# Kernel optimization log

Hardware: AMD Instinct MI355X
Metric: run time of the kernel (lower is better)

The kernel has to match this reference:

```python
import jax, jax.numpy as jnp
import numpy as np

HIDDEN, KEY_DIM, VALUE_DIM = 1024, 1024, 1024
BATCH, SEQ = 8, 2048


def setup_inputs() -> dict:
    key = jax.random.key(0)
    ks = jax.random.split(key, 9)
    s = lambda fan_in: 1.0 / np.sqrt(fan_in)
    return {
        "y_all": jax.random.normal(ks[0], (BATCH, SEQ, HIDDEN), dtype=jnp.float32),
        # torch nn.Linear weights stored as (in, out) for x @ W + b
        "Wq": jax.random.uniform(ks[1], (HIDDEN, KEY_DIM), jnp.float32, -s(HIDDEN), s(HIDDEN)),
        "bq": jax.random.uniform(ks[2], (KEY_DIM,), jnp.float32, -s(HIDDEN), s(HIDDEN)),
        "Wk": jax.random.uniform(ks[3], (HIDDEN, KEY_DIM), jnp.float32, -s(HIDDEN), s(HIDDEN)),
        "bk": jax.random.uniform(ks[4], (KEY_DIM,), jnp.float32, -s(HIDDEN), s(HIDDEN)),
        "Wv": jax.random.uniform(ks[5], (HIDDEN, VALUE_DIM), jnp.float32, -s(HIDDEN), s(HIDDEN)),
        "bv": jax.random.uniform(ks[6], (VALUE_DIM,), jnp.float32, -s(HIDDEN), s(HIDDEN)),
        "Wo": jax.random.uniform(ks[7], (VALUE_DIM, HIDDEN), jnp.float32, -s(VALUE_DIM), s(VALUE_DIM)),
        "bo": jax.random.uniform(ks[8], (HIDDEN,), jnp.float32, -s(VALUE_DIM), s(VALUE_DIM)),
    }


def reference(y_all, Wq, bq, Wk, bk, Wv, bv, Wo, bo):
    # Original loops over t, each step attending last hidden state to the full
    # prefix. Equivalent to a single causal-masked attention pass.
    B, T, H = y_all.shape
    dk = Wq.shape[1]
    q = (y_all @ Wq + bq) / jnp.sqrt(jnp.asarray(dk, y_all.dtype))  # [B,T,dk]
    k = y_all @ Wk + bk                                              # [B,T,dk]
    v = y_all @ Wv + bv                                              # [B,T,dv]
    scores = jnp.einsum("bid,bjd->bij", q, k)                        # [B,T,T]
    causal = jnp.tril(jnp.ones((T, T), dtype=bool))                  # j <= i
    scores = jnp.where(causal, scores, -jnp.inf)
    weights = jax.nn.softmax(scores, axis=-1)
    ctx = jnp.einsum("bij,bjd->bid", weights, v)                     # [B,T,dv]
    return ctx @ Wo + bo                                             # [B,T,H]
```

## Files before the change

kernel.cpp:

```cpp
#include <hip/hip_runtime.h>

typedef __attribute__((ext_vector_type(8))) __bf16 bf16x8;
typedef __attribute__((ext_vector_type(4))) float f32x4;
typedef __attribute__((ext_vector_type(4))) float f4;
typedef __attribute__((ext_vector_type(4))) unsigned short ushort4_t;

__device__ inline void gload16(const void* g, void* l) {
  __builtin_amdgcn_global_load_lds(
      (const __attribute__((address_space(1))) unsigned int*)g,
      (__attribute__((address_space(3))) unsigned int*)l, 16, 0, 0);
}

__global__ void convert_bf16_k(const float* __restrict__ in, __bf16* __restrict__ out, int n8) {
  int i = blockIdx.x * blockDim.x + threadIdx.x;
  int stride = gridDim.x * blockDim.x;
  for (; i < n8; i += stride) {
    f4 a = ((const f4*)in)[2 * (long long)i];
    f4 b = ((const f4*)in)[2 * (long long)i + 1];
    bf16x8 o;
#pragma unroll
    for (int e = 0; e < 4; e++) { o[e] = (__bf16)a[e]; o[e + 4] = (__bf16)b[e]; }
    ((bf16x8*)out)[i] = o;
  }
}

__global__ void pack_bias_k(const float* __restrict__ bq, const float* __restrict__ bk,
                            const float* __restrict__ bv, float* __restrict__ out) {
  int i = blockIdx.x * 256 + threadIdx.x;
  if (i >= 3072) return;
  const float* src = (i < 1024) ? bq : (i < 2048) ? bk : bv;
  out[i] = src[i & 1023];
}

__global__ void transpose_w_k(const float* __restrict__ W0, const float* __restrict__ W1,
                              const float* __restrict__ W2, const float* __restrict__ W3,
                              __bf16* __restrict__ out) {
  int z = blockIdx.z;
  const float* W = (z == 0) ? W0 : (z == 1) ? W1 : (z == 2) ? W2 : W3;
  __bf16* O = out + (long long)z * 1048576;
  __shared__ float tile[32][33];
  int tx = threadIdx.x, ty = threadIdx.y;
  int n0 = blockIdx.x * 32, k0 = blockIdx.y * 32;
#pragma unroll
  for (int i = 0; i < 4; i++)
    tile[ty + i * 8][tx] = W[(long long)(k0 + ty + i * 8) * 1024 + n0 + tx];
  __syncthreads();
#pragma unroll
  for (int i = 0; i < 4; i++)
    O[(long long)(n0 + ty + i * 8) * 1024 + k0 + tx] = (__bf16)tile[tx][ty + i * 8];
}


#define LOADA(BASE, MIB)                                                       \
  _Pragma("unroll") for (int mi = 0; mi < 4; mi++)                             \
      _Pragma("unroll") for (int kh = 0; kh < 2; kh++) {                       \
    int row = ((MIB) + mi) * 16 + ln15;                                        \
    int pb = (row * 128 + (kh * 32 + kq * 8) * 2) ^ ((row & 7) << 4);          \
    a[mi][kh] = *(const bf16x8*)((BASE) + pb);                                 \
  }

#define LOADB(BASE, NIB)                                                       \
  _Pragma("unroll") for (int ni = 0; ni < 2; ni++)                             \
      _Pragma("unroll") for (int kh = 0; kh < 2; kh++) {                       \
    int row = brow0 + ((NIB) + ni) * 16 + ln15;                                \
    int pb = (row * 128 + (kh * 32 + kq * 8) * 2) ^ ((row & 7) << 4);          \
    b[(NIB) + ni][kh] = *(const bf16x8*)((BASE) + pb);                         \
  }

#define MFMAQ(MI0, NI0)                                                        \
  _Pragma("unroll") for (int mi = 0; mi < 4; mi++)                             \
      _Pragma("unroll") for (int ni = 0; ni < 2; ni++)                         \
          _Pragma("unroll") for (int kh = 0; kh < 2; kh++)                     \
              acc[(MI0) + mi][(NI0) + ni] =                                    \
      __builtin_amdgcn_mfma_f32_16x16x32_bf16(a[mi][kh], b[(NI0) + ni][kh],    \
                                              acc[(MI0) + mi][(NI0) + ni], 0, 0, 0);

#define FENCE asm volatile("" ::: "memory")

#define BARW                                           \
  FENCE;                                               \
  __builtin_amdgcn_s_barrier();                        \
  FENCE;                                               \
  __builtin_amdgcn_s_setprio(1);

#define ENDP                                           \
  __builtin_amdgcn_s_setprio(0);                       \
  FENCE;                                               \
  __builtin_amdgcn_s_barrier();                        \
  FENCE;

#define ENDPB                                          \
  __builtin_amdgcn_s_setprio(0);                       \
  asm volatile("s_waitcnt vmcnt(8)" ::: "memory");     \
  __builtin_amdgcn_s_barrier();                        \
  FENCE;

template <int OUT, int SWZ>
__global__ __launch_bounds__(512, 2) void gemm8(
    const __bf16* __restrict__ A0, int lda, long long sAz,
    const __bf16* __restrict__ B0, int ldb, long long sBz,
    void* __restrict__ C0v, int ldc, long long sCz,
    const float* __restrict__ bias0, int sBiasZ,
    float scale_z0, int k_tiles_base, int k_tiles_per_br,
    __bf16* __restrict__ vt_out) {
  int br, bc, z;
  {
    const int lin = (blockIdx.z * gridDim.y + blockIdx.y) * gridDim.x + blockIdx.x;
    if (SWZ == 1) {
      const int q = lin & 7, c = lin >> 3;
      br = q * 8 + (c & 7);
      const int rest = c >> 3;
      const int nz = gridDim.z;
      z = rest % nz;
      bc = rest / nz;
    } else if (SWZ == 2) {
      const int q = lin & 7, c = lin >> 3;
      z = q;
      int b0 = (int)((sqrtf((float)(8 * c + 1)) - 1.0f) * 0.5f);
      int c0 = c - ((b0 * (b0 + 1)) >> 1);
      if (c0 < 0) { b0--; c0 = c - ((b0 * (b0 + 1)) >> 1); }
      if (c0 > b0) { b0++; c0 = c - ((b0 * (b0 + 1)) >> 1); }
      br = b0;
      bc = c0;
    } else if (SWZ == 3) {
      const int q = lin & 7, c = lin >> 3;
      z = q;
      br = c & 7;
      bc = c >> 3;
    } else {
      const int nbx = gridDim.x, nby = gridDim.y;
      const int nwg = nbx * nby * gridDim.z;
      const int cpx = nwg >> 3;
      const int swz = (lin & 7) * cpx + (lin >> 3);
      br = swz % nbx;
      const int tmp = swz / nbx;
      bc = tmp % nby;
      z = tmp / nby;
    }
  }
  const int kt = k_tiles_base + k_tiles_per_br * br;

  __shared__ __align__(16) __bf16 lds[81920];

  const int t = threadIdx.x, w = t >> 6, lane = t & 63;
  const int wm = w >> 2, wn = w & 3;
  const int ln15 = lane & 15, kq = lane >> 4;
  const int bh = wn >> 1, brow0 = (wn & 1) * 64;

  const __bf16* A = A0 + (long long)z * sAz + (long long)br * 256 * lda;
  const __bf16* B = B0 + (long long)z * sBz + (long long)bc * 256 * ldb;

  int r0s[2], c0s[2];
#pragma unroll
  for (int i = 0; i < 2; i++) {
    int o = i * 8192 + t * 16;
    int lo = o ^ (((o >> 7) & 7) << 4);
    r0s[i] = lo >> 7;
    c0s[i] = (lo & 127) >> 1;
  }
  const __bf16 *sA0[2], *sA1[2], *sB0[2], *sB1[2];
#pragma unroll
  for (int i = 0; i < 2; i++) {
    sA0[i] = A + (long long)r0s[i] * lda + c0s[i];
    sA1[i] = A + (long long)(r0s[i] + 128) * lda + c0s[i];
    sB0[i] = B + (long long)r0s[i] * ldb + c0s[i];
    sB1[i] = B + (long long)(r0s[i] + 128) * ldb + c0s[i];
  }

  auto stg = [&](const __bf16* const* src, __bf16* lbase, int g) {
    int kc = g < kt ? g : kt - 1;
#pragma unroll
    for (int i = 0; i < 2; i++)
      gload16(src[i] + kc * 64, lbase + i * 4096 + w * 512);
  };

  f32x4 acc[8][4] = {};
  bf16x8 a[4][2], b[4][2];

  stg(sA0, lds, 0);
  stg(sA1, lds + 8192, 0);
  stg(sB0, lds + 49152, 0);
  stg(sB1, lds + 49152 + 8192, 0);
  stg(sA0, lds + 16384, 1);
  stg(sA1, lds + 16384 + 8192, 1);
  stg(sB0, lds + 65536, 1);
  stg(sB1, lds + 65536 + 8192, 1);
  asm volatile("s_waitcnt vmcnt(8)" ::: "memory");
  __builtin_amdgcn_s_barrier();
  FENCE;

  int ap = 0;
  int ad = 2;
  for (int kk = 0; kk < kt; kk++) {
    __bf16* Ab = lds + ap * 16384;
    __bf16* Bb = lds + 49152 + (kk & 1) * 16384;
    __bf16* Ad = lds + ad * 16384;
    __bf16* Bd = Bb;
    const char* Aw = (const char*)(Ab + wm * 8192);
    const char* Bw = (const char*)(Bb + bh * 8192);
    LOADA(Aw, 0) LOADB(Bw, 0)
    stg(sA0, Ad, kk + 2);
    BARW MFMAQ(0, 0) ENDP
    LOADB(Bw, 2)
    stg(sA1, Ad + 8192, kk + 2);
    BARW MFMAQ(0, 2) ENDP
    LOADA(Aw, 4)
    stg(sB0, Bd, kk + 2);
    BARW MFMAQ(4, 2) ENDP
    stg(sB1, Bd + 8192, kk + 2);
    BARW MFMAQ(4, 0) ENDPB
    ap = (ap == 2) ? 0 : ap + 1;
    ad = (ad == 2) ? 0 : ad + 1;
  }

  if (OUT == 2 && z == 2) {
    __syncthreads();
    char* lb = (char*)lds;
    const int dl0 = wn * 64 + ln15;
    const int tl0 = wm * 128 + kq * 4;
#pragma unroll
    for (int mi = 0; mi < 8; mi++) {
#pragma unroll
      for (int ni = 0; ni < 4; ni++) {
        const int d = dl0 + ni * 16;
        const int tl = tl0 + mi * 16;
        const float bb = bias0[2048 + bc * 256 + d];
        ushort4_t p;
#pragma unroll
        for (int j = 0; j < 4; j++) {
          union { __bf16 h; unsigned short u; } cv;
          cv.h = (__bf16)(acc[mi][ni][j] + bb);
          p[j] = cv.u;
        }
        int byte = d * 512 + tl * 2;
        byte ^= (d & 7) << 4;
        *(ushort4_t*)(lb + byte) = p;
      }
    }
    __syncthreads();
    const int bz = br >> 3;
    __bf16* vbase = vt_out + (long long)bz * 2097152 +
                    (long long)(bc * 256) * 2048 + (br & 7) * 256;
#pragma unroll
    for (int it = 0; it < 16; it++) {
      int idx = it * 512 + t;
      int d = idx >> 5, tc = idx & 31;
      int byte = d * 512 + tc * 16;
      byte ^= (d & 7) << 4;
      bf16x8 vv = *(const bf16x8*)(lb + byte);
      *(bf16x8*)(vbase + (long long)d * 2048 + tc * 8) = vv;
    }
  } else {
    const int row0 = br * 256 + wm * 128 + kq * 4;
    const int col0 = bc * 256 + wn * 64 + ln15;
    const float scale = (z == 0) ? scale_z0 : 1.0f;
    const float* bias = bias0 ? (bias0 + (long long)z * sBiasZ) : nullptr;
#pragma unroll
    for (int mi = 0; mi < 8; mi++) {
#pragma unroll
      for (int ni = 0; ni < 4; ni++) {
        const int rr = row0 + mi * 16;
        const int cc = col0 + ni * 16;
        const float bb = bias ? bias[cc] : 0.0f;
#pragma unroll
        for (int j = 0; j < 4; j++) {
          float v = (acc[mi][ni][j] + bb) * scale;
          long long off = (long long)z * sCz + (long long)(rr + j) * ldc + cc;
          if (OUT == 1)
            ((float*)C0v)[off] = v;
          else
            ((__bf16*)C0v)[off] = (__bf16)v;
        }
      }
    }
  }
}

__global__ __launch_bounds__(256) void softmax_rows(__bf16* __restrict__ S) {
  const int row = blockIdx.x;
  const int i = row & 2047;
  __bf16* s = S + (long long)row * 2048;
  const int Lpad = (i + 256) & ~255;
  const int t = threadIdx.x;
  const int j0 = t * 8;
  const int wid = t >> 6, lane = t & 63;
  const bool active = j0 < Lpad;

  float v[8];
  float mymax = -3.0e38f;
  if (active) {
    bf16x8 x = *(const bf16x8*)(s + j0);
#pragma unroll
    for (int e = 0; e < 8; e++) {
      float f = (float)x[e];
      v[e] = ((j0 + e) <= i) ? f : -3.0e38f;
      mymax = fmaxf(mymax, v[e]);
    }
  }
  float mw = mymax;
#pragma unroll
  for (int o = 32; o >= 1; o >>= 1) mw = fmaxf(mw, __shfl_xor(mw, o));
  __shared__ float redm[4];
  __shared__ float reds[4];
  if (lane == 0) redm[wid] = mw;
  __syncthreads();
  const float m = fmaxf(fmaxf(redm[0], redm[1]), fmaxf(redm[2], redm[3]));

  float e8[8];
  float mysum = 0.0f;
  if (active) {
#pragma unroll
    for (int e = 0; e < 8; e++) {
      float ev = ((j0 + e) <= i) ? __expf(v[e] - m) : 0.0f;
      e8[e] = ev;
      mysum += ev;
    }
  } else {
#pragma unroll
    for (int e = 0; e < 8; e++) e8[e] = 0.0f;
  }
  float sw = mysum;
#pragma unroll
  for (int o = 32; o >= 1; o >>= 1) sw += __shfl_xor(sw, o);
  if (lane == 0) reds[wid] = sw;
  __syncthreads();
  const float l = reds[0] + reds[1] + reds[2] + reds[3];
  const float rl = 1.0f / l;
  if (active) {
    bf16x8 o;
#pragma unroll
    for (int e = 0; e < 8; e++) o[e] = (__bf16)(e8[e] * rl);
    *(bf16x8*)(s + j0) = o;
  }
}

extern "C" void kernel_launch(void* const* d_in, const int* in_sizes, int n_in,
                              void* d_out, int out_size, void* d_ws, size_t ws_size,
                              hipStream_t stream) {
  const float* y  = (const float*)d_in[0];
  const float* Wq = (const float*)d_in[1];
  const float* bq = (const float*)d_in[2];
  const float* Wk = (const float*)d_in[3];
  const float* bk = (const float*)d_in[4];
  const float* Wv = (const float*)d_in[5];
  const float* bv = (const float*)d_in[6];
  const float* Wo = (const float*)d_in[7];
  const float* bo = (const float*)d_in[8];

  char* ws = (char*)d_ws;
  __bf16* Xb   = (__bf16*)(ws + 0);
  __bf16* Wt   = (__bf16*)(ws + 33554432);
  float*  bqkv = (float*)(ws + 41943040);
  __bf16* Qb   = (__bf16*)(ws + 41955328);
  __bf16* Kb   = (__bf16*)(ws + 75509760);
  __bf16* Vt   = (__bf16*)(ws + 109064192);
  __bf16* Sb   = (__bf16*)(ws + 142618624);
  __bf16* ctx  = (__bf16*)(ws + 0);

  if (ws_size < 209727488u) return;

  convert_bf16_k<<<2048, 256, 0, stream>>>(y, Xb, 2097152);
  pack_bias_k<<<12, 256, 0, stream>>>(bq, bk, bv, bqkv);
  transpose_w_k<<<dim3(32, 32, 4), dim3(32, 8), 0, stream>>>(Wq, Wk, Wv, Wo, Wt);

  gemm8<2, 1><<<dim3(64, 4, 3), 512, 0, stream>>>(
      Xb, 1024, 0LL, Wt, 1024, 1048576LL,
      Qb, 1024, 16777216LL, bqkv, 1024, 0.03125f, 16, 0, Vt);

  gemm8<0, 2><<<dim3(36, 1, 8), 512, 0, stream>>>(
      Qb, 1024, 2097152LL, Kb, 1024, 2097152LL,
      Sb, 2048, 4194304LL, nullptr, 0, 1.0f, 16, 0, nullptr);

  softmax_rows<<<16384, 256, 0, stream>>>(Sb);

  gemm8<0, 3><<<dim3(8, 4, 8), 512, 0, stream>>>(
      Sb, 2048, 4194304LL, Vt, 2048, 2097152LL,
      ctx, 1024, 2097152LL, nullptr, 0, 1.0f, 4, 4, nullptr);

  gemm8<1, 1><<<dim3(64, 4, 1), 512, 0, stream>>>(
      ctx, 1024, 0LL, Wt + 3 * 1048576, 1024, 0LL,
      d_out, 1024, 0LL, bo, 0, 1.0f, 16, 0, nullptr);
}
```

Measured before the change: 317.1 us.

## Peel last k-tile to overlap epilogue stores with final MFMAs; reorder SWZ1 mapping

The last k-iteration of the GEMM main loop is peeled out and runs without barriers or further staging. Each quarter of the output tile is stored right after its MFMA group, so global stores overlap with the remaining matrix math instead of waiting for a separate epilogue. Separately, the SWZ==1 block mapping now iterates bc before z, which changes which tiles run concurrently and their L2 locality. This adds code size and register pressure, and depends on the peeled loop still handling the triple-buffer indices correctly.

```diff
diff --git a/kernel.cpp b/kernel.cpp
--- a/kernel.cpp
+++ b/kernel.cpp
@@ -74,6 +74,22 @@
               acc[(MI0) + mi][(NI0) + ni] =                                    \
       __builtin_amdgcn_mfma_f32_16x16x32_bf16(a[mi][kh], b[(NI0) + ni][kh],    \
                                               acc[(MI0) + mi][(NI0) + ni], 0, 0, 0);
+
+#define STOREQ(MI0, NI0)                                                       \
+  if (OUT != 2 || z < 2) {                                                     \
+    _Pragma("unroll") for (int mi = 0; mi < 4; mi++)                           \
+        _Pragma("unroll") for (int ni = 0; ni < 2; ni++) {                     \
+      const int rr = row0 + ((MI0) + mi) * 16;                                 \
+      const int cc = col0 + ((NI0) + ni) * 16;                                 \
+      const float bb = bias ? bias[cc] : 0.0f;                                 \
+      _Pragma("unroll") for (int j = 0; j < 4; j++) {                          \
+        float vv = (acc[(MI0) + mi][(NI0) + ni][j] + bb) * scale;              \
+        long long off = (long long)z * sCz + (long long)(rr + j) * ldc + cc;   \
+        if (OUT == 1) ((float*)C0v)[off] = vv;                                 \
+        else ((__bf16*)C0v)[off] = (__bf16)vv;                                 \
+      }                                                                        \
+    }                                                                          \
+  }
 
 #define FENCE asm volatile("" ::: "memory")
 
@@ -110,9 +126,9 @@
       const int q = lin & 7, c = lin >> 3;
       br = q * 8 + (c & 7);
       const int rest = c >> 3;
-      const int nz = gridDim.z;
-      z = rest % nz;
-      bc = rest / nz;
+      const int nby = gridDim.y;
+      bc = rest % nby;
+      z = rest / nby;
     } else if (SWZ == 2) {
       const int q = lin & 7, c = lin >> 3;
       z = q;
@@ -177,6 +193,11 @@
   f32x4 acc[8][4] = {};
   bf16x8 a[4][2], b[4][2];
 
+  const int row0 = br * 256 + wm * 128 + kq * 4;
+  const int col0 = bc * 256 + wn * 64 + ln15;
+  const float scale = (z == 0) ? scale_z0 : 1.0f;
+  const float* bias = bias0 ? (bias0 + (long long)z * sBiasZ) : nullptr;
+
   stg(sA0, lds, 0);
   stg(sA1, lds + 8192, 0);
   stg(sB0, lds + 49152, 0);
@@ -191,7 +212,7 @@
 
   int ap = 0;
   int ad = 2;
-  for (int kk = 0; kk < kt; kk++) {
+  for (int kk = 0; kk < kt - 1; kk++) {
     __bf16* Ab = lds + ap * 16384;
     __bf16* Bb = lds + 49152 + (kk & 1) * 16384;
     __bf16* Ad = lds + ad * 16384;
@@ -213,6 +234,25 @@
     ad = (ad == 2) ? 0 : ad + 1;
   }
 
+  {
+    __bf16* Ab = lds + ap * 16384;
+    __bf16* Bb = lds + 49152 + ((kt - 1) & 1) * 16384;
+    const char* Aw = (const char*)(Ab + wm * 8192);
+    const char* Bw = (const char*)(Bb + bh * 8192);
+    LOADA(Aw, 0) LOADB(Bw, 0) LOADB(Bw, 2)
+    __builtin_amdgcn_s_setprio(1);
+    MFMAQ(0, 0)
+    STOREQ(0, 0)
+    MFMAQ(0, 2)
+    STOREQ(0, 2)
+    LOADA(Aw, 4)
+    MFMAQ(4, 2)
+    STOREQ(4, 2)
+    MFMAQ(4, 0)
+    __builtin_amdgcn_s_setprio(0);
+    STOREQ(4, 0)
+  }
+
   if (OUT == 2 && z == 2) {
     __syncthreads();
     char* lb = (char*)lds;
@@ -250,29 +290,6 @@
       bf16x8 vv = *(const bf16x8*)(lb + byte);
       *(bf16x8*)(vbase + (long long)d * 2048 + tc * 8) = vv;
     }
-  } else {
-    const int row0 = br * 256 + wm * 128 + kq * 4;
-    const int col0 = bc * 256 + wn * 64 + ln15;
-    const float scale = (z == 0) ? scale_z0 : 1.0f;
-    const float* bias = bias0 ? (bias0 + (long long)z * sBiasZ) : nullptr;
-#pragma unroll
-    for (int mi = 0; mi < 8; mi++) {
-#pragma unroll
-      for (int ni = 0; ni < 4; ni++) {
-        const int rr = row0 + mi * 16;
-        const int cc = col0 + ni * 16;
-        const float bb = bias ? bias[cc] : 0.0f;
-#pragma unroll
-        for (int j = 0; j < 4; j++) {
-          float v = (acc[mi][ni][j] + bb) * scale;
-          long long off = (long long)z * sCz + (long long)(rr + j) * ldc + cc;
-          if (OUT == 1)
-            ((float*)C0v)[off] = v;
-          else
-            ((__bf16*)C0v)[off] = (__bf16)v;
-        }
-      }
-    }
   }
 }
 
```

Result: no change. 314.6 us (-0.8%).

## Use smaller 128x128-tile GEMM kernel for causal QK^T and PV stages

Applied to the files above, without the earlier changes.

Adds a 256-thread gemm4 kernel with 128x128 tiles and a simple single-buffered LDS loop. It replaces the 256-tile gemm8 for the triangular QK^T scores and the causal-limited PV product. The finer tiles cut the work wasted on masked regions and give more workgroups for occupancy. The cost is less data reuse per tile, and the loads are no longer overlapped with the MFMA compute.

```diff
diff --git a/kernel.cpp b/kernel.cpp
--- a/kernel.cpp
+++ b/kernel.cpp
@@ -110,23 +110,9 @@
       const int q = lin & 7, c = lin >> 3;
       br = q * 8 + (c & 7);
       const int rest = c >> 3;
-      const int nz = gridDim.z;
-      z = rest % nz;
-      bc = rest / nz;
-    } else if (SWZ == 2) {
-      const int q = lin & 7, c = lin >> 3;
-      z = q;
-      int b0 = (int)((sqrtf((float)(8 * c + 1)) - 1.0f) * 0.5f);
-      int c0 = c - ((b0 * (b0 + 1)) >> 1);
-      if (c0 < 0) { b0--; c0 = c - ((b0 * (b0 + 1)) >> 1); }
-      if (c0 > b0) { b0++; c0 = c - ((b0 * (b0 + 1)) >> 1); }
-      br = b0;
-      bc = c0;
-    } else if (SWZ == 3) {
-      const int q = lin & 7, c = lin >> 3;
-      z = q;
-      br = c & 7;
-      bc = c >> 3;
+      const int nby = gridDim.y;
+      bc = rest % nby;
+      z = rest / nby;
     } else {
       const int nbx = gridDim.x, nby = gridDim.y;
       const int nwg = nbx * nby * gridDim.z;
@@ -276,6 +262,106 @@
   }
 }
 
+template <int TRI>
+__global__ __launch_bounds__(256, 3) void gemm4(
+    const __bf16* __restrict__ A0, int lda, long long sAz,
+    const __bf16* __restrict__ B0, int ldb, long long sBz,
+    __bf16* __restrict__ C0, int ldc, long long sCz,
+    int k_tiles_base, int k_tiles_per_br) {
+  int br, bc, z;
+  if (TRI) {
+    const int c = blockIdx.x;
+    z = blockIdx.y;
+    int b0 = (int)((sqrtf((float)(8 * c + 1)) - 1.0f) * 0.5f);
+    int c0 = c - ((b0 * (b0 + 1)) >> 1);
+    if (c0 < 0) { b0--; c0 = c - ((b0 * (b0 + 1)) >> 1); }
+    if (c0 > b0) { b0++; c0 = c - ((b0 * (b0 + 1)) >> 1); }
+    br = b0;
+    bc = c0;
+  } else {
+    br = blockIdx.x;
+    bc = blockIdx.y;
+    z = blockIdx.z;
+  }
+  const int kt = k_tiles_base + k_tiles_per_br * br;
+
+  __shared__ __align__(16) __bf16 lds[16384];
+
+  const int t = threadIdx.x, w = t >> 6, lane = t & 63;
+  const int wm = w >> 1, wn = w & 1;
+  const int ln15 = lane & 15, kq = lane >> 4;
+
+  const __bf16* A = A0 + (long long)z * sAz + (long long)br * 128 * lda;
+  const __bf16* B = B0 + (long long)z * sBz + (long long)bc * 128 * ldb;
+
+  const __bf16 *sA[4], *sB[4];
+#pragma unroll
+  for (int i = 0; i < 4; i++) {
+    int o = i * 4096 + t * 16;
+    int lo = o ^ (((o >> 7) & 7) << 4);
+    int r = lo >> 7, c = (lo & 127) >> 1;
+    sA[i] = A + (long long)r * lda + c;
+    sB[i] = B + (long long)r * ldb + c;
+  }
+
+  f32x4 acc[4][4] = {};
+
+  for (int kk = 0; kk < kt; kk++) {
+#pragma unroll
+    for (int i = 0; i < 4; i++)
+      gload16(sA[i] + kk * 64, lds + i * 2048 + w * 512);
+#pragma unroll
+    for (int i = 0; i < 4; i++)
+      gload16(sB[i] + kk * 64, lds + 8192 + i * 2048 + w * 512);
+    asm volatile("s_waitcnt vmcnt(0)" ::: "memory");
+    __builtin_amdgcn_s_barrier();
+    FENCE;
+    const char* Ab = (const char*)lds;
+    const char* Bb = (const char*)(lds + 8192);
+    __builtin_amdgcn_s_setprio(1);
+#pragma unroll
+    for (int kh = 0; kh < 2; kh++) {
+      bf16x8 a[4], b[4];
+#pragma unroll
+      for (int mi = 0; mi < 4; mi++) {
+        int row = wm * 64 + mi * 16 + ln15;
+        int pb = (row * 128 + (kh * 32 + kq * 8) * 2) ^ ((row & 7) << 4);
+        a[mi] = *(const bf16x8*)(Ab + pb);
+      }
+#pragma unroll
+      for (int ni = 0; ni < 4; ni++) {
+        int row = wn * 64 + ni * 16 + ln15;
+        int pb = (row * 128 + (kh * 32 + kq * 8) * 2) ^ ((row & 7) << 4);
+        b[ni] = *(const bf16x8*)(Bb + pb);
+      }
+#pragma unroll
+      for (int mi = 0; mi < 4; mi++)
+#pragma unroll
+        for (int ni = 0; ni < 4; ni++)
+          acc[mi][ni] = __builtin_amdgcn_mfma_f32_16x16x32_bf16(
+              a[mi], b[ni], acc[mi][ni], 0, 0, 0);
+    }
+    __builtin_amdgcn_s_setprio(0);
+    FENCE;
+    __builtin_amdgcn_s_barrier();
+    FENCE;
+  }
+
+  const int row0 = br * 128 + wm * 64 + kq * 4;
+  const int col0 = bc * 128 + wn * 64 + ln15;
+#pragma unroll
+  for (int mi = 0; mi < 4; mi++) {
+#pragma unroll
+    for (int ni = 0; ni < 4; ni++) {
+      const int rr = row0 + mi * 16, cc = col0 + ni * 16;
+#pragma unroll
+      for (int j = 0; j < 4; j++)
+        C0[(long long)z * sCz + (long long)(rr + j) * ldc + cc] =
+            (__bf16)acc[mi][ni][j];
+    }
+  }
+}
+
 __global__ __launch_bounds__(256) void softmax_rows(__bf16* __restrict__ S) {
   const int row = blockIdx.x;
   const int i = row & 2047;
@@ -367,15 +453,15 @@
       Xb, 1024, 0LL, Wt, 1024, 1048576LL,
       Qb, 1024, 16777216LL, bqkv, 1024, 0.03125f, 16, 0, Vt);
 
-  gemm8<0, 2><<<dim3(36, 1, 8), 512, 0, stream>>>(
+  gemm4<1><<<dim3(136, 8, 1), 256, 0, stream>>>(
       Qb, 1024, 2097152LL, Kb, 1024, 2097152LL,
-      Sb, 2048, 4194304LL, nullptr, 0, 1.0f, 16, 0, nullptr);
+      Sb, 2048, 4194304LL, 16, 0);
 
   softmax_rows<<<16384, 256, 0, stream>>>(Sb);
 
-  gemm8<0, 3><<<dim3(8, 4, 8), 512, 0, stream>>>(
+  gemm4<0><<<dim3(16, 8, 8), 256, 0, stream>>>(
       Sb, 2048, 4194304LL, Vt, 2048, 2097152LL,
-      ctx, 1024, 2097152LL, nullptr, 0, 1.0f, 4, 4, nullptr);
+      ctx, 1024, 2097152LL, 2, 2);
 
   gemm8<1, 1><<<dim3(64, 4, 1), 512, 0, stream>>>(
       ctx, 1024, 0LL, Wt + 3 * 1048576, 1024, 0LL,
```

Measured after the change: 342.5 us. 1.08x slower.
